# Kernel optimization log

Hardware: AMD Instinct MI355X
Metric: run time of the kernel (lower is better)

The kernel has to match this reference:

```python
import jax, jax.numpy as jnp
import numpy as np

N = 4096
IN_SIZE = 512
MLP_W = 16
HID = 512
MID = 64  # hardcoded tgc2 output size in the torch module
OUT = 128
BN_EPS = 1e-5


def setup_inputs() -> dict:
    key = jax.random.key(0)
    ks = jax.random.split(key, 24)
    adj = (jax.random.uniform(ks[0], (N, N)) < 0.05).astype(jnp.float32)
    xdeg = jax.random.uniform(ks[1], (N, N), dtype=jnp.float32)
    ydeg = jax.random.uniform(ks[2], (N, N), dtype=jnp.float32)
    u = lambda k, sh, fan: jax.random.uniform(k, sh, jnp.float32, -1.0, 1.0) / np.sqrt(fan)
    return {
        "adj": adj, "xdeg": xdeg, "ydeg": ydeg,
        # edge MLP: 3 -> MLP_W -> 2
        "mlp_w1": u(ks[3], (3, MLP_W), 3), "mlp_b1": jnp.zeros((MLP_W,), jnp.float32),
        "mlp_w2": u(ks[4], (MLP_W, 2), MLP_W), "mlp_b2": jnp.zeros((2,), jnp.float32),
        # positional linear: Linear(N, in_size) applied to eye(N) -> pe = W^T + b
        "pe_w": u(ks[5], (N, IN_SIZE), N), "pe_b": jnp.zeros((IN_SIZE,), jnp.float32),
        # GCN weights
        "gc1_w": u(ks[6], (IN_SIZE, HID), HID),
        "lin2_w": u(ks[7], (HID, MID), HID), "lin2_b": jnp.zeros((MID,), jnp.float32),
        "gc3_w": u(ks[8], (MID, OUT), OUT),
        # BatchNorm (eval mode: running stats)
        "bn1_g": jnp.ones((HID,), jnp.float32), "bn1_b": jnp.zeros((HID,), jnp.float32),
        "bn1_m": jnp.zeros((HID,), jnp.float32), "bn1_v": jnp.ones((HID,), jnp.float32),
        "bn2_g": jnp.ones((OUT,), jnp.float32), "bn2_b": jnp.zeros((OUT,), jnp.float32),
        "bn2_m": jnp.zeros((OUT,), jnp.float32), "bn2_v": jnp.ones((OUT,), jnp.float32),
    }


def reference(adj, xdeg, ydeg, mlp_w1, mlp_b1, mlp_w2, mlp_b2, pe_w, pe_b,
              gc1_w, lin2_w, lin2_b, gc3_w,
              bn1_g, bn1_b, bn1_m, bn1_v, bn2_g, bn2_b, bn2_m, bn2_v):
    # Edge MLP + softmax over [adj, xdeg, ydeg] features; torch only computes it
    # at nonzero adj entries then scatters into a dense mask. Since the mask is
    # multiplied by adj, computing densely and multiplying is exactly equivalent.
    feats = jnp.stack([adj, xdeg, ydeg], axis=-1)          # [N, N, 3]
    h = jax.nn.relu(jnp.einsum('nmf,fw->nmw', feats, mlp_w1) + mlp_b1)
    logits = jnp.einsum('nmw,wc->nmc', h, mlp_w2) + mlp_b2  # [N, N, 2]
    mask = jax.nn.softmax(logits, axis=-1)[..., 1]          # [N, N]
    a = adj * mask + jnp.eye(adj.shape[0], dtype=adj.dtype)

    # Degree normalization: A' = D_row^{-1/2} A D_col^{-1/2} (broadcast, no diag matmuls)
    rowsum = jnp.sum(a, axis=1)
    colsum = jnp.sum(a, axis=0)
    d_row = jnp.where(rowsum > 0, rowsum ** -0.5, 0.0)
    d_col = jnp.where(colsum > 0, colsum ** -0.5, 0.0)
    a = d_row[:, None] * a * d_col[None, :]

    # pe = Linear(eye(N)) = W^T + b (eval mode, dropout off)
    pe = pe_w + pe_b[None, :]                               # [N, IN_SIZE]

    h = a @ (pe @ gc1_w)                                    # GCN layer 1
    h = (h - bn1_m) * (bn1_g / jnp.sqrt(bn1_v + BN_EPS)) + bn1_b
    h = h @ lin2_w + lin2_b                                 # tgc2
    mid = h
    h = jax.nn.relu(h)
    h = a @ (h @ gc3_w)                                     # GCN layer 3
    out = (h - bn2_m) * (bn2_g / jnp.sqrt(bn2_v + BN_EPS)) + bn2_b
    return out, mid
```

## Files before the change

kernel.cpp:

```cpp
#include <hip/hip_runtime.h>
#include <hip/hip_bf16.h>

#define NN 4096
#define INS 512
#define HIDW 512
#define MIDW 64
#define OUTW 128
#define CAP 384
#define SEG 96
#define BN_EPS 1e-5f
#define CS_BLOCKS 256
#define CS_ROWS (NN / CS_BLOCKS)
#define NSTRIP 8
#define SLOTCAP (NSTRIP * SEG)

__global__ __launch_bounds__(256) void k_count(
    const float* __restrict__ adj,
    int* __restrict__ cslot, int* __restrict__ cnt, int* __restrict__ dflag)
{
    const int t = threadIdx.x;
    const int wave = t >> 6, lane = t & 63;
    const int gw = blockIdx.x * 4 + wave;
    const int i = gw >> 3, s = gw & 7;
    const int colbase = s * 512;
    const float* __restrict__ base = adj + (size_t)i * NN + colbase + 4 * lane;
    float4 a4a = *reinterpret_cast<const float4*>(base);
    float4 a4b = *reinterpret_cast<const float4*>(base + 256);
    const float av[8] = {a4a.x, a4a.y, a4a.z, a4a.w,
                         a4b.x, a4b.y, a4b.z, a4b.w};
    int* __restrict__ slot = cslot + (size_t)i * SLOTCAP + s * SEG;
    const unsigned long long lt = (1ULL << lane) - 1ULL;
    int run = 0;
    #pragma unroll
    for (int c = 0; c < 8; ++c) {
        int col = colbase + ((c < 4) ? (4 * lane + c) : (256 + 4 * lane + c - 4));
        bool diag = (col == i);
        bool act = (av[c] != 0.f) || diag;
        if (diag) dflag[i] = (av[c] != 0.f) ? 1 : 0;
        unsigned long long m = __ballot(act);
        if (act) {
            int pos = run + __popcll(m & lt);
            if (pos < SEG) slot[pos] = col;
        }
        run += __popcll(m);
    }
    if (lane == 0) cnt[gw] = (run < SEG) ? run : SEG;
}

__global__ __launch_bounds__(256) void k_fill(
    const float* __restrict__ xdeg, const float* __restrict__ ydeg,
    const int* __restrict__ cslot, const int* __restrict__ cnt,
    const int* __restrict__ dflag,
    const float* __restrict__ w1, const float* __restrict__ b1,
    const float* __restrict__ w2, const float* __restrict__ b2,
    float* __restrict__ a_vals, int* __restrict__ a_cols,
    float* __restrict__ rs_part)
{
    __shared__ float shb[16], sw1x[16], sw1y[16], sw2[32], sb2[2];
    const int t = threadIdx.x;
    const int wave = t >> 6, lane = t & 63;
    if (t < 16) {
        shb[t]  = b1[t] + w1[t];
        sw1x[t] = w1[16 + t];
        sw1y[t] = w1[32 + t];
    }
    if (t < 32) sw2[t] = w2[t];
    if (t < 2)  sb2[t] = b2[t];
    __syncthreads();

    const int gw = __builtin_amdgcn_readfirstlane(blockIdx.x * 4 + wave);
    const int i = gw >> 3, s = gw & 7;
    const int* __restrict__ cb = cnt + i * NSTRIP;
    int wb = 0;
    #pragma unroll
    for (int ss = 0; ss < NSTRIP; ++ss) if (ss < s) wb += cb[ss];
    const int n = cb[s];
    const int hasde = dflag[i];
    const int* __restrict__ slot = cslot + (size_t)i * SLOTCAP + s * SEG;
    const float* __restrict__ xrow = xdeg + (size_t)i * NN;
    const float* __restrict__ yrow = ydeg + (size_t)i * NN;
    float* __restrict__ gv = a_vals + (size_t)i * CAP;
    int*   __restrict__ gc = a_cols + (size_t)i * CAP;

    float local = 0.f;
    for (int p = lane; p < n; p += 64) {
        int col = slot[p];
        float x = xrow[col];
        float y = yrow[col];
        float l0 = sb2[0], l1 = sb2[1];
        #pragma unroll
        for (int w = 0; w < 16; ++w) {
            float hw = fmaf(x, sw1x[w], shb[w]);
            hw = fmaf(y, sw1y[w], hw);
            hw = fmaxf(hw, 0.f);
            l0 = fmaf(hw, sw2[2 * w],     l0);
            l1 = fmaf(hw, sw2[2 * w + 1], l1);
        }
        float v = 1.f / (1.f + __expf(l0 - l1));
        if (col == i) v = hasde ? (v + 1.f) : 1.f;
        int gp = wb + p;
        if (gp < CAP) { gc[gp] = col; gv[gp] = v; }
        local += v;
    }
    #pragma unroll
    for (int o = 32; o >= 1; o >>= 1)
        local += __shfl_down(local, o, 64);
    if (lane == 0) rs_part[gw] = local;
}

__global__ __launch_bounds__(256) void k_colsum(
    const float* __restrict__ a_vals, const int* __restrict__ a_cols,
    const int* __restrict__ cnt, float* __restrict__ P)
{
    __shared__ float ls[NN];
    const int t = threadIdx.x;
    const int b = blockIdx.x;
    for (int j = t; j < NN; j += 256) ls[j] = 0.f;
    __syncthreads();
    const int r0 = b * CS_ROWS;
    for (int r = r0; r < r0 + CS_ROWS; ++r) {
        int n = 0;
        #pragma unroll
        for (int ss = 0; ss < NSTRIP; ++ss) n += cnt[r * NSTRIP + ss];
        n = (n < CAP) ? n : CAP;
        const float* __restrict__ vr = a_vals + (size_t)r * CAP;
        const int*   __restrict__ cr = a_cols + (size_t)r * CAP;
        for (int p = t; p < n; p += 256)
            atomicAdd(&ls[cr[p]], vr[p]);
    }
    __syncthreads();
    for (int j = t; j < NN; j += 256)
        P[(size_t)b * NN + j] = ls[j];
}

__global__ __launch_bounds__(512) void k_misc(
    const float* __restrict__ lin2_w, const float* __restrict__ lin2_b,
    const float* __restrict__ bn1_g, const float* __restrict__ bn1_b,
    const float* __restrict__ bn1_m, const float* __restrict__ bn1_v,
    const float* __restrict__ bn2_g, const float* __restrict__ bn2_b,
    const float* __restrict__ bn2_m, const float* __restrict__ bn2_v,
    const float* __restrict__ rs_part, const float* __restrict__ P,
    float* __restrict__ Wp, float* __restrict__ c1,
    float* __restrict__ s2g, float* __restrict__ t2g,
    float* __restrict__ d_row, float* __restrict__ d_col)
{
    const int t = threadIdx.x;
    if (blockIdx.x == 0) {
        __shared__ float t1s[HIDW];
        {
            int h = t;
            float s1 = bn1_g[h] * rsqrtf(bn1_v[h] + BN_EPS);
            t1s[h] = bn1_b[h] - bn1_m[h] * s1;
            for (int m = 0; m < MIDW; ++m)
                Wp[(size_t)h * MIDW + m] = s1 * lin2_w[(size_t)h * MIDW + m];
        }
        __syncthreads();
        if (t < MIDW) {
            float acc = lin2_b[t];
            for (int h = 0; h < HIDW; ++h)
                acc = fmaf(t1s[h], lin2_w[(size_t)h * MIDW + t], acc);
            c1[t] = acc;
        } else if (t >= 64 && t < 64 + OUTW) {
            int j = t - 64;
            float s2 = bn2_g[j] * rsqrtf(bn2_v[j] + BN_EPS);
            s2g[j] = s2;
            t2g[j] = bn2_b[j] - bn2_m[j] * s2;
        }
    } else {
        int j = (blockIdx.x - 1) * 512 + t;
        float r = 0.f;
        #pragma unroll
        for (int s = 0; s < NSTRIP; ++s) r += rs_part[j * NSTRIP + s];
        d_row[j] = (r > 0.f) ? 1.f / sqrtf(r) : 0.f;
        float c = 0.f;
        for (int b = 0; b < CS_BLOCKS; ++b)
            c += P[(size_t)b * NN + j];
        d_col[j] = (c > 0.f) ? 1.f / sqrtf(c) : 0.f;
    }
}

template <bool ABIAS, bool ROWSCALE>
__global__ __launch_bounds__(256) void k_thin(
    const float* __restrict__ A, const float* __restrict__ B,
    const float* __restrict__ abias, const float* __restrict__ rscale,
    float* __restrict__ C, int M, int K)
{
    __shared__ float As[64][36];
    __shared__ float Bs[64][64];
    const int t = threadIdx.x;
    const int bm = blockIdx.x * 32;
    const int c2 = t & 31, rg = t >> 5;

    float acc[4][2] = {};

    for (int k0 = 0; k0 < K; k0 += 64) {
        #pragma unroll
        for (int l = 0; l < 8; ++l) {
            int e = t + l * 256;
            int r = e >> 6, k = e & 63;
            float v = A[(size_t)(bm + r) * K + k0 + k];
            if (ABIAS) v += abias[k0 + k];
            As[k][r] = v;
        }
        #pragma unroll
        for (int l = 0; l < 16; ++l) {
            int e = t + l * 256;
            int k = e >> 6, n = e & 63;
            Bs[k][n] = B[(size_t)(k0 + k) * 64 + n];
        }
        __syncthreads();
        #pragma unroll
        for (int k = 0; k < 64; ++k) {
            float4 a4 = *reinterpret_cast<const float4*>(&As[k][rg * 4]);
            float2 b2 = *reinterpret_cast<const float2*>(&Bs[k][2 * c2]);
            acc[0][0] = fmaf(a4.x, b2.x, acc[0][0]);
            acc[0][1] = fmaf(a4.x, b2.y, acc[0][1]);
            acc[1][0] = fmaf(a4.y, b2.x, acc[1][0]);
            acc[1][1] = fmaf(a4.y, b2.y, acc[1][1]);
            acc[2][0] = fmaf(a4.z, b2.x, acc[2][0]);
            acc[2][1] = fmaf(a4.z, b2.y, acc[2][1]);
            acc[3][0] = fmaf(a4.w, b2.x, acc[3][0]);
            acc[3][1] = fmaf(a4.w, b2.y, acc[3][1]);
        }
        __syncthreads();
    }

    #pragma unroll
    for (int u = 0; u < 4; ++u) {
        int r = bm + rg * 4 + u;
        float sc = ROWSCALE ? rscale[r] : 1.f;
        float2 o = make_float2(acc[u][0] * sc, acc[u][1] * sc);
        *reinterpret_cast<float2*>(&C[(size_t)r * 64 + 2 * c2]) = o;
    }
}

template <bool WITH_MID>
__global__ __launch_bounds__(256) void k_spmm(
    const float* __restrict__ a_vals, const int* __restrict__ a_cols,
    const int* __restrict__ cnt, const float* __restrict__ X,
    const float* __restrict__ d_row, const float* __restrict__ d_col,
    const float* __restrict__ c1,
    const float* __restrict__ gc3, const float* __restrict__ s2g,
    const float* __restrict__ t2g,
    float* __restrict__ O1, float* __restrict__ O2)
{
    __shared__ float sv[2][CAP];
    __shared__ int   scl[2][CAP];
    __shared__ float sacc[4][64];
    const int t = threadIdx.x;
    const int wave = t >> 6, lane = t & 63;
    const int rb = wave >> 1, h = wave & 1;
    const int i = blockIdx.x * 2 + rb;
    int n = 0;
    #pragma unroll
    for (int ss = 0; ss < NSTRIP; ++ss) n += cnt[i * NSTRIP + ss];
    n = (n < CAP) ? n : CAP;
    const int n16 = (n + 15) & ~15;
    const float* __restrict__ vrow = a_vals + (size_t)i * CAP;
    const int*   __restrict__ crow = a_cols + (size_t)i * CAP;

    for (int p = h * 64 + lane; p < n16; p += 128) {
        bool ok = p < n;
        sv[rb][p]  = ok ? vrow[p] : 0.f;
        scl[rb][p] = ok ? crow[p] : 0;
    }
    __syncthreads();

    const int eh = lane >> 5;
    const int lc = lane & 31;
    const int Q  = n16 >> 1;
    const int Qh = Q >> 1;

    float a0 = 0.f, a1 = 0.f;
    for (int q = h * Qh; q < (h + 1) * Qh; q += 4) {
        #pragma unroll
        for (int j = 0; j < 4; ++j) {
            int p = 2 * (q + j) + eh;
            float v = sv[rb][p];
            int c = scl[rb][p];
            float2 x = *reinterpret_cast<const float2*>(X + (size_t)c * 64 + 2 * lc);
            a0 = fmaf(v, x.x, a0);
            a1 = fmaf(v, x.y, a1);
        }
    }
    a0 += __shfl_xor(a0, 32);
    a1 += __shfl_xor(a1, 32);
    if (lane < 32) { sacc[wave][2 * lc] = a0; sacc[wave][2 * lc + 1] = a1; }
    __syncthreads();

    if (WITH_MID) {
        if (h == 0 && lane < 32) {
            float s0 = sacc[wave][2 * lc]     + sacc[wave + 1][2 * lc];
            float s1 = sacc[wave][2 * lc + 1] + sacc[wave + 1][2 * lc + 1];
            float dr = d_row[i];
            float dc = d_col[i];
            float m0 = fmaf(s0, dr, c1[2 * lc]);
            float m1 = fmaf(s1, dr, c1[2 * lc + 1]);
            *reinterpret_cast<float2*>(O1 + (size_t)i * 64 + 2 * lc) =
                make_float2(m0, m1);
            *reinterpret_cast<float2*>(O2 + (size_t)i * 64 + 2 * lc) =
                make_float2(dc * fmaxf(m0, 0.f), dc * fmaxf(m1, 0.f));
        }
    } else {
        if (h == 0 && lane < 32) {
            float dr = d_row[i];
            float s0 = (sacc[wave][2 * lc]     + sacc[wave + 1][2 * lc])     * dr;
            float s1 = (sacc[wave][2 * lc + 1] + sacc[wave + 1][2 * lc + 1]) * dr;
            sacc[wave][2 * lc]     = s0;
            sacc[wave][2 * lc + 1] = s1;
        }
        __syncthreads();
        const int rb2 = t >> 7;
        const int j = t & 127;
        const float* __restrict__ srow = sacc[2 * rb2];
        float acc = 0.f;
        #pragma unroll 8
        for (int k = 0; k < 64; ++k)
            acc = fmaf(srow[k], gc3[k * 128 + j], acc);
        int orow = blockIdx.x * 2 + rb2;
        O1[(size_t)orow * 128 + j] = fmaf(acc, s2g[j], t2g[j]);
    }
}

extern "C" void kernel_launch(void* const* d_in, const int* in_sizes, int n_in,
                              void* d_out, int out_size, void* d_ws, size_t ws_size,
                              hipStream_t stream) {
    const float* adj    = (const float*)d_in[0];
    const float* xdeg   = (const float*)d_in[1];
    const float* ydeg   = (const float*)d_in[2];
    const float* mlp_w1 = (const float*)d_in[3];
    const float* mlp_b1 = (const float*)d_in[4];
    const float* mlp_w2 = (const float*)d_in[5];
    const float* mlp_b2 = (const float*)d_in[6];
    const float* pe_w   = (const float*)d_in[7];
    const float* pe_b   = (const float*)d_in[8];
    const float* gc1_w  = (const float*)d_in[9];
    const float* lin2_w = (const float*)d_in[10];
    const float* lin2_b = (const float*)d_in[11];
    const float* gc3_w  = (const float*)d_in[12];
    const float* bn1_g  = (const float*)d_in[13];
    const float* bn1_b  = (const float*)d_in[14];
    const float* bn1_m  = (const float*)d_in[15];
    const float* bn1_v  = (const float*)d_in[16];
    const float* bn2_g  = (const float*)d_in[17];
    const float* bn2_b  = (const float*)d_in[18];
    const float* bn2_m  = (const float*)d_in[19];
    const float* bn2_v  = (const float*)d_in[20];

    float* out = (float*)d_out;
    float* mid = out + (size_t)NN * OUTW;

    char* w = (char*)d_ws;
    float* a_vals = (float*)w;  w += (size_t)NN * CAP * 4;
    int*   a_cols = (int*)w;    w += (size_t)NN * CAP * 4;
    int*   cslot  = (int*)w;    w += (size_t)NN * SLOTCAP * 4;
    int*   cnt    = (int*)w;    w += (size_t)NN * NSTRIP * 4;
    int*   dflag  = (int*)w;    w += (size_t)NN * 4;
    float* rs_part= (float*)w;  w += (size_t)NN * NSTRIP * 4;
    float* d_row  = (float*)w;  w += (size_t)NN * 4;
    float* d_col  = (float*)w;  w += (size_t)NN * 4;
    float* P      = (float*)w;  w += (size_t)CS_BLOCKS * NN * 4;
    float* Wp     = (float*)w;  w += (size_t)HIDW * MIDW * 4;
    float* W2     = (float*)w;  w += (size_t)INS * MIDW * 4;
    float* c1     = (float*)w;  w += 256;
    float* s2g    = (float*)w;  w += 512;
    float* t2g    = (float*)w;  w += 512;
    float* G      = (float*)w;  w += (size_t)NN * MIDW * 4;
    float* R      = (float*)w;  w += (size_t)NN * MIDW * 4;

    k_count<<<NN * NSTRIP / 4, 256, 0, stream>>>(adj, cslot, cnt, dflag);
    k_fill<<<NN * NSTRIP / 4, 256, 0, stream>>>(
        xdeg, ydeg, cslot, cnt, dflag, mlp_w1, mlp_b1, mlp_w2, mlp_b2,
        a_vals, a_cols, rs_part);
    k_colsum<<<CS_BLOCKS, 256, 0, stream>>>(a_vals, a_cols, cnt, P);
    k_misc<<<9, 512, 0, stream>>>(lin2_w, lin2_b, bn1_g, bn1_b, bn1_m, bn1_v,
                                  bn2_g, bn2_b, bn2_m, bn2_v, rs_part, P,
                                  Wp, c1, s2g, t2g, d_row, d_col);
    k_thin<false, false><<<INS / 32, 256, 0, stream>>>(
        gc1_w, Wp, nullptr, nullptr, W2, INS, HIDW);
    k_thin<true, true><<<NN / 32, 256, 0, stream>>>(
        pe_w, W2, pe_b, d_col, G, NN, INS);
    k_spmm<true><<<NN / 2, 256, 0, stream>>>(
        a_vals, a_cols, cnt, G, d_row, d_col, c1,
        nullptr, nullptr, nullptr, mid, R);
    k_spmm<false><<<NN / 2, 256, 0, stream>>>(
        a_vals, a_cols, cnt, R, d_row, d_col, nullptr,
        gc3_w, s2g, t2g, out, nullptr);
}
```

Measured before the change: 137.4 us.

## Fuse adjacency count and edge-MLP fill into one kernel with strip-padded CSR

Merges the nonzero-compaction pass and the edge-MLP value pass into a single kernel. Column indices now stay in shared memory instead of going through a global slot buffer, and the separate diagonal-flag array is replaced by a per-wave ballot. Values and columns are stored per strip at fixed offsets, so no prefix sum over strip counts is needed in the producer. The column-sum and SpMM kernels now walk the strip segments and compact them while loading, which adds some index bookkeeping on the consumer side.

```diff
diff --git a/kernel.cpp b/kernel.cpp
--- a/kernel.cpp
+++ b/kernel.cpp
@@ -14,13 +14,28 @@
 #define NSTRIP 8
 #define SLOTCAP (NSTRIP * SEG)
 
-__global__ __launch_bounds__(256) void k_count(
-    const float* __restrict__ adj,
-    int* __restrict__ cslot, int* __restrict__ cnt, int* __restrict__ dflag)
-{
+__global__ __launch_bounds__(256) void k_build(
+    const float* __restrict__ adj, const float* __restrict__ xdeg,
+    const float* __restrict__ ydeg,
+    const float* __restrict__ w1, const float* __restrict__ b1,
+    const float* __restrict__ w2, const float* __restrict__ b2,
+    float* __restrict__ a_vals, int* __restrict__ a_cols,
+    int* __restrict__ cnt, float* __restrict__ rs_part)
+{
+    __shared__ float shb[16], sw1x[16], sw1y[16], sw2[32], sb2[2];
+    __shared__ int   scol[4][SEG];
     const int t = threadIdx.x;
     const int wave = t >> 6, lane = t & 63;
-    const int gw = blockIdx.x * 4 + wave;
+    if (t < 16) {
+        shb[t]  = b1[t] + w1[t];
+        sw1x[t] = w1[16 + t];
+        sw1y[t] = w1[32 + t];
+    }
+    if (t < 32) sw2[t] = w2[t];
+    if (t < 2)  sb2[t] = b2[t];
+    __syncthreads();
+
+    const int gw = __builtin_amdgcn_readfirstlane(blockIdx.x * 4 + wave);
     const int i = gw >> 3, s = gw & 7;
     const int colbase = s * 512;
     const float* __restrict__ base = adj + (size_t)i * NN + colbase + 4 * lane;
@@ -28,63 +43,33 @@
     float4 a4b = *reinterpret_cast<const float4*>(base + 256);
     const float av[8] = {a4a.x, a4a.y, a4a.z, a4a.w,
                          a4b.x, a4b.y, a4b.z, a4b.w};
-    int* __restrict__ slot = cslot + (size_t)i * SLOTCAP + s * SEG;
     const unsigned long long lt = (1ULL << lane) - 1ULL;
     int run = 0;
+    bool hasde = false;
     #pragma unroll
     for (int c = 0; c < 8; ++c) {
         int col = colbase + ((c < 4) ? (4 * lane + c) : (256 + 4 * lane + c - 4));
         bool diag = (col == i);
-        bool act = (av[c] != 0.f) || diag;
-        if (diag) dflag[i] = (av[c] != 0.f) ? 1 : 0;
+        bool nz = (av[c] != 0.f);
+        bool act = nz || diag;
+        unsigned long long md = __ballot(nz && diag);
+        if (md) hasde = true;
         unsigned long long m = __ballot(act);
         if (act) {
             int pos = run + __popcll(m & lt);
-            if (pos < SEG) slot[pos] = col;
+            if (pos < SEG) scol[wave][pos] = col;
         }
         run += __popcll(m);
     }
-    if (lane == 0) cnt[gw] = (run < SEG) ? run : SEG;
-}
-
-__global__ __launch_bounds__(256) void k_fill(
-    const float* __restrict__ xdeg, const float* __restrict__ ydeg,
-    const int* __restrict__ cslot, const int* __restrict__ cnt,
-    const int* __restrict__ dflag,
-    const float* __restrict__ w1, const float* __restrict__ b1,
-    const float* __restrict__ w2, const float* __restrict__ b2,
-    float* __restrict__ a_vals, int* __restrict__ a_cols,
-    float* __restrict__ rs_part)
-{
-    __shared__ float shb[16], sw1x[16], sw1y[16], sw2[32], sb2[2];
-    const int t = threadIdx.x;
-    const int wave = t >> 6, lane = t & 63;
-    if (t < 16) {
-        shb[t]  = b1[t] + w1[t];
-        sw1x[t] = w1[16 + t];
-        sw1y[t] = w1[32 + t];
-    }
-    if (t < 32) sw2[t] = w2[t];
-    if (t < 2)  sb2[t] = b2[t];
-    __syncthreads();
-
-    const int gw = __builtin_amdgcn_readfirstlane(blockIdx.x * 4 + wave);
-    const int i = gw >> 3, s = gw & 7;
-    const int* __restrict__ cb = cnt + i * NSTRIP;
-    int wb = 0;
-    #pragma unroll
-    for (int ss = 0; ss < NSTRIP; ++ss) if (ss < s) wb += cb[ss];
-    const int n = cb[s];
-    const int hasde = dflag[i];
-    const int* __restrict__ slot = cslot + (size_t)i * SLOTCAP + s * SEG;
+    const int n = (run < SEG) ? run : SEG;
+
     const float* __restrict__ xrow = xdeg + (size_t)i * NN;
     const float* __restrict__ yrow = ydeg + (size_t)i * NN;
-    float* __restrict__ gv = a_vals + (size_t)i * CAP;
-    int*   __restrict__ gc = a_cols + (size_t)i * CAP;
-
+    float* __restrict__ gv = a_vals + (size_t)i * SLOTCAP + s * SEG;
+    int*   __restrict__ gc = a_cols + (size_t)i * SLOTCAP + s * SEG;
     float local = 0.f;
     for (int p = lane; p < n; p += 64) {
-        int col = slot[p];
+        int col = scol[wave][p];
         float x = xrow[col];
         float y = yrow[col];
         float l0 = sb2[0], l1 = sb2[1];
@@ -98,14 +83,14 @@
         }
         float v = 1.f / (1.f + __expf(l0 - l1));
         if (col == i) v = hasde ? (v + 1.f) : 1.f;
-        int gp = wb + p;
-        if (gp < CAP) { gc[gp] = col; gv[gp] = v; }
+        gc[p] = col;
+        gv[p] = v;
         local += v;
     }
     #pragma unroll
     for (int o = 32; o >= 1; o >>= 1)
         local += __shfl_down(local, o, 64);
-    if (lane == 0) rs_part[gw] = local;
+    if (lane == 0) { rs_part[gw] = local; cnt[gw] = n; }
 }
 
 __global__ __launch_bounds__(256) void k_colsum(
@@ -119,14 +104,14 @@
     __syncthreads();
     const int r0 = b * CS_ROWS;
     for (int r = r0; r < r0 + CS_ROWS; ++r) {
-        int n = 0;
-        #pragma unroll
-        for (int ss = 0; ss < NSTRIP; ++ss) n += cnt[r * NSTRIP + ss];
-        n = (n < CAP) ? n : CAP;
-        const float* __restrict__ vr = a_vals + (size_t)r * CAP;
-        const int*   __restrict__ cr = a_cols + (size_t)r * CAP;
-        for (int p = t; p < n; p += 256)
-            atomicAdd(&ls[cr[p]], vr[p]);
+        const float* __restrict__ vr = a_vals + (size_t)r * SLOTCAP;
+        const int*   __restrict__ cr = a_cols + (size_t)r * SLOTCAP;
+        #pragma unroll
+        for (int ss = 0; ss < NSTRIP; ++ss) {
+            int ns = cnt[r * NSTRIP + ss];
+            for (int p = t; p < ns; p += 256)
+                atomicAdd(&ls[cr[ss * SEG + p]], vr[ss * SEG + p]);
+        }
     }
     __syncthreads();
     for (int j = t; j < NN; j += 256)
@@ -250,20 +235,29 @@
     const int t = threadIdx.x;
     const int wave = t >> 6, lane = t & 63;
     const int rb = wave >> 1, h = wave & 1;
-    const int i = blockIdx.x * 2 + rb;
-    int n = 0;
+    const int i = __builtin_amdgcn_readfirstlane(blockIdx.x * 2 + rb);
+    const float* __restrict__ vrow = a_vals + (size_t)i * SLOTCAP;
+    const int*   __restrict__ crow = a_cols + (size_t)i * SLOTCAP;
+
+    int run = 0;
     #pragma unroll
-    for (int ss = 0; ss < NSTRIP; ++ss) n += cnt[i * NSTRIP + ss];
-    n = (n < CAP) ? n : CAP;
+    for (int ss = 0; ss < NSTRIP; ++ss) {
+        int ns = cnt[i * NSTRIP + ss];
+        if ((ss & 1) == h) {
+            for (int p = lane; p < ns; p += 64) {
+                int pos = run + p;
+                if (pos < CAP) {
+                    sv[rb][pos]  = vrow[ss * SEG + p];
+                    scl[rb][pos] = crow[ss * SEG + p];
+                }
+            }
+        }
+        run += ns;
+    }
+    const int n = (run < CAP) ? run : CAP;
     const int n16 = (n + 15) & ~15;
-    const float* __restrict__ vrow = a_vals + (size_t)i * CAP;
-    const int*   __restrict__ crow = a_cols + (size_t)i * CAP;
-
-    for (int p = h * 64 + lane; p < n16; p += 128) {
-        bool ok = p < n;
-        sv[rb][p]  = ok ? vrow[p] : 0.f;
-        scl[rb][p] = ok ? crow[p] : 0;
-    }
+    for (int p = h * 64 + lane; p < n16; p += 128)
+        if (p >= n) { sv[rb][p] = 0.f; scl[rb][p] = 0; }
     __syncthreads();
 
     const int eh = lane >> 5;
@@ -351,11 +345,9 @@
     float* mid = out + (size_t)NN * OUTW;
 
     char* w = (char*)d_ws;
-    float* a_vals = (float*)w;  w += (size_t)NN * CAP * 4;
-    int*   a_cols = (int*)w;    w += (size_t)NN * CAP * 4;
-    int*   cslot  = (int*)w;    w += (size_t)NN * SLOTCAP * 4;
+    float* a_vals = (float*)w;  w += (size_t)NN * SLOTCAP * 4;
+    int*   a_cols = (int*)w;    w += (size_t)NN * SLOTCAP * 4;
     int*   cnt    = (int*)w;    w += (size_t)NN * NSTRIP * 4;
-    int*   dflag  = (int*)w;    w += (size_t)NN * 4;
     float* rs_part= (float*)w;  w += (size_t)NN * NSTRIP * 4;
     float* d_row  = (float*)w;  w += (size_t)NN * 4;
     float* d_col  = (float*)w;  w += (size_t)NN * 4;
@@ -368,10 +360,9 @@
     float* G      = (float*)w;  w += (size_t)NN * MIDW * 4;
     float* R      = (float*)w;  w += (size_t)NN * MIDW * 4;
 
-    k_count<<<NN * NSTRIP / 4, 256, 0, stream>>>(adj, cslot, cnt, dflag);
-    k_fill<<<NN * NSTRIP / 4, 256, 0, stream>>>(
-        xdeg, ydeg, cslot, cnt, dflag, mlp_w1, mlp_b1, mlp_w2, mlp_b2,
-        a_vals, a_cols, rs_part);
+    k_build<<<NN * NSTRIP / 4, 256, 0, stream>>>(
+        adj, xdeg, ydeg, mlp_w1, mlp_b1, mlp_w2, mlp_b2,
+        a_vals, a_cols, cnt, rs_part);
     k_colsum<<<CS_BLOCKS, 256, 0, stream>>>(a_vals, a_cols, cnt, P);
     k_misc<<<9, 512, 0, stream>>>(lin2_w, lin2_b, bn1_g, bn1_b, bn1_m, bn1_v,
                                   bn2_g, bn2_b, bn2_m, bn2_v, rs_part, P,
```

New measurement: 162.9 us. +18.5%, slower.
